# Kernel tuning notes

Hardware: AMD Instinct MI355X
Metric: run time of the kernel (lower is better)

## Reference

```python
import jax, jax.numpy as jnp
import numpy as np

BATCH_K = 8
CUTOFF = 0.5
NONZERO_LOSS_CUTOFF = 1.4
N, D = 8192, 128


def setup_inputs() -> dict:
    key = jax.random.key(0)
    x = jax.random.normal(key, (N, D), dtype=jnp.float32)
    # the sqrt(2 - 2*sim) distance assumes unit-norm embeddings
    x = x / jnp.linalg.norm(x, axis=1, keepdims=True)
    return {"x": x}


def _forward(x, key):
    n, d = x.shape
    k = BATCH_K
    # pairwise distances on the unit sphere
    sim = x @ x.T                                   # [n, n]
    dist = jnp.sqrt(jnp.maximum(2.0 - 2.0 * sim, 0.0))
    # clamp distance from below at cutoff (canonical distance-weighted sampling;
    # repo's clamp(max=) + torch.maxx are typos that make the original code NaN/crash)
    dist = jnp.maximum(dist, CUTOFF)
    one_minus = jnp.maximum(1.0 - 0.25 * dist * dist, 1e-8)  # tiny clip for log safety
    log_w = (2.0 - float(d)) * jnp.log(dist) - (float(d - 3) / 2.0) * jnp.log(one_minus)
    w = jnp.exp(log_w - jnp.max(log_w))
    # zero out the same-class (block-diagonal) entries and far pairs
    blk = jnp.arange(n) // k
    neq_block = (blk[:, None] != blk[None, :]).astype(x.dtype)
    w = w * neq_block * (dist < NONZERO_LOSS_CUTOFF).astype(x.dtype)
    row_sum = jnp.sum(w, axis=1, keepdims=True)
    # uniform fallback for degenerate rows (mirrors the try/except in the original)
    probs = jnp.where(row_sum > 0, w / row_sum, 1.0 / n)   # [n, n]
    # per-row categorical sampling of k-1 negatives WITH replacement
    logits = jnp.log(probs)                                # -inf where prob==0 (ok)
    n_idx = jax.random.categorical(key, logits, shape=(k - 1, n)).T.reshape(-1)  # [n*(k-1)]
    # anchor/positive pairs: all same-block pairs (i, j), j != i
    a_idx = jnp.repeat(jnp.arange(n), k - 1)               # [n*(k-1)]
    p_mat = blk[:, None] * k + jnp.arange(k)[None, :]      # [n, k]
    keep = p_mat != jnp.arange(n)[:, None]
    order = jnp.argsort(jnp.logical_not(keep), axis=1, stable=True)
    p_idx = jnp.take_along_axis(p_mat, order, axis=1)[:, : k - 1].reshape(-1)
    return a_idx, x[a_idx], x[p_idx], x[n_idx], x


def reference(x):
    return _forward(x, jax.random.key(1))
```

## Files before the change

kernel.cpp:

```cpp
#include <hip/hip_runtime.h>

#define NN   8192
#define DD   128
#define KM1  7
#define TPB  256
#define NBLK 512

#define O0_END   57344
#define O1_END   7397376
#define O2_END   14737408
#define O3_END   22077440
#define TOTAL    23126016
#define NKEY     57344

typedef __attribute__((ext_vector_type(8))) short bf16x8;
typedef __attribute__((ext_vector_type(4))) float f32x4;

__device__ __forceinline__ unsigned mix32(unsigned h) {
  h ^= h >> 16; h *= 0x85ebca6bu; h ^= h >> 13; h *= 0xc2b2ae35u; h ^= h >> 16;
  return h;
}

__device__ __forceinline__ float wfun(float dot, int col, int rowblk) {
  float d2m = fmaxf(fmaf(-2.f, dot, 2.f), 0.25f);
  bool vb = ((col >> 3) != rowblk) && (d2m < 1.96f);
  float lgd = __log2f(d2m);
  float om  = fmaf(-0.25f, d2m, 1.f);
  float lgo = __log2f(om);
  float lgw = fmaf(-62.5f, lgo, fmaf(-63.f, lgd, -63.f));
  float w   = __builtin_amdgcn_exp2f(lgw);
  return vb ? w : 0.f;
}

__device__ __forceinline__ float wave_incl_scan(float v, int lane) {
#pragma unroll
  for (int off = 1; off < 64; off <<= 1) {
    float t = __shfl_up(v, off);
    if (lane >= off) v += t;
  }
  return v;
}

__global__ __launch_bounds__(256) void to_bf16(const float4* __restrict__ x4,
                                               ushort4* __restrict__ xb4) {
  const int i = blockIdx.x * 256 + threadIdx.x;
  float4 v = x4[i];
  ushort4 o;
  unsigned u;
  u = __float_as_uint(v.x); o.x = (unsigned short)((u + 0x7FFFu + ((u >> 16) & 1u)) >> 16);
  u = __float_as_uint(v.y); o.y = (unsigned short)((u + 0x7FFFu + ((u >> 16) & 1u)) >> 16);
  u = __float_as_uint(v.z); o.z = (unsigned short)((u + 0x7FFFu + ((u >> 16) & 1u)) >> 16);
  u = __float_as_uint(v.w); o.w = (unsigned short)((u + 0x7FFFu + ((u >> 16) & 1u)) >> 16);
  xb4[i] = o;
}

__global__ __launch_bounds__(TPB, 2) void pass_a(const unsigned short* __restrict__ xb,
                                                 float* __restrict__ bs) {
  const int tid  = threadIdx.x;
  const int lane = tid & 63;
  const int wid  = tid >> 6;
  const int l15  = lane & 15;
  const int g    = lane >> 4;
  const int i0   = ((int)(blockIdx.x >> 5)) * 256 + wid * 64;
  const int oc   = (int)(blockIdx.x & 31);
  const int c0   = oc * 256;
  const int koff = g * 8;

  bf16x8 rw[4][4];
#pragma unroll
  for (int rg = 0; rg < 4; ++rg) {
    const unsigned short* rp = xb + (size_t)(i0 + rg * 16 + l15) * DD + koff;
#pragma unroll
    for (int kk = 0; kk < 4; ++kk)
      rw[rg][kk] = *reinterpret_cast<const bf16x8*>(rp + kk * 32);
  }

  float bsl[16];
#pragma unroll
  for (int j = 0; j < 16; ++j) bsl[j] = 0.f;

#pragma unroll 1
  for (int t = 0; t < 8; ++t) {
    const int ct = c0 + t * 32;
    bf16x8 cf[2][4];
#pragma unroll
    for (int mf = 0; mf < 2; ++mf) {
      const unsigned short* cp = xb + (size_t)(ct + mf * 16 + l15) * DD + koff;
#pragma unroll
      for (int kk = 0; kk < 4; ++kk)
        cf[mf][kk] = *reinterpret_cast<const bf16x8*>(cp + kk * 32);
    }

    f32x4 acc[2][4];
#pragma unroll
    for (int mf = 0; mf < 2; ++mf)
#pragma unroll
      for (int rg = 0; rg < 4; ++rg) acc[mf][rg] = (f32x4){0.f, 0.f, 0.f, 0.f};

#pragma unroll
    for (int mf = 0; mf < 2; ++mf)
#pragma unroll
      for (int rg = 0; rg < 4; ++rg)
#pragma unroll
        for (int kk = 0; kk < 4; ++kk)
          acc[mf][rg] = __builtin_amdgcn_mfma_f32_16x16x32_bf16(cf[mf][kk], rw[rg][kk],
                                                                acc[mf][rg], 0, 0, 0);

#pragma unroll
    for (int mf = 0; mf < 2; ++mf) {
      float s[4];
#pragma unroll
      for (int rg = 0; rg < 4; ++rg) {
        const int rowblk = (i0 + rg * 16 + l15) >> 3;
        float sv = 0.f;
#pragma unroll
        for (int r = 0; r < 4; ++r) {
          const int col = ct + mf * 16 + g * 4 + r;
          sv += wfun(acc[mf][rg][r], col, rowblk);
        }
        sv += __shfl_xor(sv, 16);
        sv += __shfl_xor(sv, 32);
        s[rg] = sv;
      }
      float v = (g == 0) ? s[0] : (g == 1) ? s[1] : (g == 2) ? s[2] : s[3];
      bsl[2 * t + mf] = v;
    }
  }

  float* dst = bs + (size_t)(i0 + lane) * NBLK + oc * 16;
#pragma unroll
  for (int k4 = 0; k4 < 4; ++k4) {
    f32x4 o = {bsl[4 * k4], bsl[4 * k4 + 1], bsl[4 * k4 + 2], bsl[4 * k4 + 3]};
    *reinterpret_cast<f32x4*>(dst + 4 * k4) = o;
  }
}

__global__ __launch_bounds__(TPB) void pass_b(const unsigned short* __restrict__ xb,
                                              const float* __restrict__ bs,
                                              unsigned* __restrict__ nidx) {
  const int lane = threadIdx.x & 63;
  const int wid  = threadIdx.x >> 6;
  const int draw = (int)blockIdx.x * 4 + wid;
  const int row  = draw / KM1;

  const float* bsr = bs + (size_t)row * NBLK;
  float4 v0 = *reinterpret_cast<const float4*>(bsr + lane * 8);
  float4 v1 = *reinterpret_cast<const float4*>(bsr + lane * 8 + 4);
  float s8 = ((v0.x + v0.y) + (v0.z + v0.w)) + ((v1.x + v1.y) + (v1.z + v1.w));
  float pre = wave_incl_scan(s8, lane);
  float W = __shfl(pre, 63);

  unsigned h = mix32((unsigned)draw * 2654435761u + 0x12345u);
  float u = ((float)(h >> 9) + 0.5f) * (1.0f / 8388608.0f);

  if (!(W > 0.f)) {
    if (lane == 0) nidx[draw] = mix32((unsigned)draw * 0x68bc21ebu + 77u) & (NN - 1);
    return;
  }
  float target = u * W;

  unsigned long long ball = __ballot(pre >= target);
  int Lc = ball ? ((int)__ffsll(ball) - 1) : 63;
  float exL = __shfl(pre - s8, Lc);
  float a0 = __shfl(v0.x, Lc), a1 = __shfl(v0.y, Lc), a2 = __shfl(v0.z, Lc),
        a3 = __shfl(v0.w, Lc), a4 = __shfl(v1.x, Lc), a5 = __shfl(v1.y, Lc),
        a6 = __shfl(v1.z, Lc), a7 = __shfl(v1.w, Lc);
  int k = -1; float res = 0.f, bsb = 0.f, c = exL;
#define PICK(j, aj) { float cn = c + (aj); if (k < 0 && cn >= target) { k = j; res = target - c; bsb = (aj); } c = cn; }
  PICK(0, a0) PICK(1, a1) PICK(2, a2) PICK(3, a3)
  PICK(4, a4) PICK(5, a5) PICK(6, a6) PICK(7, a7)
#undef PICK
#define LASTP(j, aj) { if (k < 0 && (aj) > 0.f) { k = j; res = (aj); bsb = (aj); } }
  LASTP(7, a7) LASTP(6, a6) LASTP(5, a5) LASTP(4, a4)
  LASTP(3, a3) LASTP(2, a2) LASTP(1, a1) LASTP(0, a0)
#undef LASTP
  if (k < 0) {
    if (lane == 0) nidx[draw] = mix32((unsigned)draw * 0x68bc21ebu + 77u) & (NN - 1);
    return;
  }
  const int blk = Lc * 8 + k;
  const int cb  = blk * 16;

  const int c_local = lane >> 2;
  const int part    = lane & 3;
  const int col     = cb + c_local;
  const unsigned short* cp = xb + (size_t)col * DD + part * 32;
  const unsigned short* ap = xb + (size_t)row * DD + part * 32;
  float dot = 0.f;
#pragma unroll
  for (int vv = 0; vv < 4; ++vv) {
    bf16x8 cv = *reinterpret_cast<const bf16x8*>(cp + vv * 8);
    bf16x8 av = *reinterpret_cast<const bf16x8*>(ap + vv * 8);
#pragma unroll
    for (int j = 0; j < 8; ++j) {
      float cf = __uint_as_float(((unsigned)(unsigned short)cv[j]) << 16);
      float af = __uint_as_float(((unsigned)(unsigned short)av[j]) << 16);
      dot = fmaf(cf, af, dot);
    }
  }
  dot += __shfl_xor(dot, 1);
  dot += __shfl_xor(dot, 2);
  float w = wfun(dot, col, row >> 3);
  float v = (part == 0) ? w : 0.f;
  float pre2 = wave_incl_scan(v, lane);
  float SW = __shfl(pre2, 63);
  unsigned result;
  if (SW > 0.f) {
    float t2 = (res / bsb) * SW;
    unsigned long long m = __ballot((v > 0.f) && (pre2 >= t2));
    if (m) result = (unsigned)(cb + (((int)__ffsll(m) - 1) >> 2));
    else {
      unsigned long long m2 = __ballot(v > 0.f);
      result = (unsigned)(cb + ((63 - (int)__clzll(m2)) >> 2));
    }
  } else {
    result = mix32((unsigned)draw * 0x68bc21ebu + 77u) & (NN - 1);
  }
  if (lane == 0) nidx[draw] = result;
}

__global__ __launch_bounds__(256) void write_outputs(const float* __restrict__ x,
                                                     const unsigned* __restrict__ nidx,
                                                     float* __restrict__ out) {
  const int qq = blockIdx.x * 256 + threadIdx.x;
  if (qq >= TOTAL / 4) return;
  const int e = qq * 4;
  float4 v;
  if (e < O0_END) {
    v.x = (float)((e    ) / KM1);
    v.y = (float)((e + 1) / KM1);
    v.z = (float)((e + 2) / KM1);
    v.w = (float)((e + 3) / KM1);
  } else if (e < O1_END) {
    int t = e - O0_END; int sidx = t >> 7; int d = t & 127;
    v = *reinterpret_cast<const float4*>(x + (size_t)(sidx / KM1) * DD + d);
  } else if (e < O2_END) {
    int t = e - O1_END; int sidx = t >> 7; int d = t & 127;
    int i = sidx / KM1; int j = sidx - i * KM1; int m = i & 7;
    int p = (i >> 3) * 8 + j + (j >= m ? 1 : 0);
    v = *reinterpret_cast<const float4*>(x + (size_t)p * DD + d);
  } else if (e < O3_END) {
    int t = e - O2_END; int sidx = t >> 7; int d = t & 127;
    int nix = (int)nidx[sidx];
    v = *reinterpret_cast<const float4*>(x + (size_t)nix * DD + d);
  } else {
    v = *reinterpret_cast<const float4*>(x + (e - O3_END));
  }
  f32x4 nv = {v.x, v.y, v.z, v.w};
  __builtin_nontemporal_store(nv, reinterpret_cast<f32x4*>(out + e));
}

extern "C" void kernel_launch(void* const* d_in, const int* in_sizes, int n_in,
                              void* d_out, int out_size, void* d_ws, size_t ws_size,
                              hipStream_t stream) {
  const float* x = (const float*)d_in[0];
  float* out = (float*)d_out;

  float* bs = (float*)d_ws;
  unsigned* nidx = (unsigned*)((char*)d_ws + (size_t)NN * NBLK * 4);
  unsigned short* xb = (unsigned short*)((char*)nidx + NKEY * 4);

  hipLaunchKernelGGL(to_bf16, dim3(NN * DD / 4 / 256), dim3(256), 0, stream,
                     (const float4*)x, (ushort4*)xb);
  hipLaunchKernelGGL(pass_a, dim3(1024), dim3(TPB), 0, stream, xb, bs);
  hipLaunchKernelGGL(pass_b, dim3(NKEY / 4), dim3(TPB), 0, stream, xb, bs, nidx);
  hipLaunchKernelGGL(write_outputs, dim3(TOTAL / 4 / 256), dim3(256), 0, stream,
                     x, nidx, out);
}
```

Before: 113.1 us.

## Exploit Gram-matrix symmetry in pass_a by computing only upper-triangular tile pairs

pass_a now enumerates only the upper-triangular pairs of 128-row chunks (2080 blocks) instead of every row/column tile. Each off-diagonal tile writes its row-direction block sums directly and also reduces the column-direction sums through shuffles and shared memory, then writes them transposed for the mirrored tile. This roughly halves the MFMA work and the weight-function evaluations, at the cost of extra shuffle reductions, a shared-memory transpose, a barrier and a serial loop that decodes the block index into a tile pair.

Measured after the change: 128.6 us. 1.14x slower.

```diff
diff --git a/kernel.cpp b/kernel.cpp
--- a/kernel.cpp
+++ b/kernel.cpp
@@ -5,6 +5,9 @@
 #define KM1  7
 #define TPB  256
 #define NBLK 512
+#define CH   128
+#define NCH  64
+#define NPAIR 2080
 
 #define O0_END   57344
 #define O1_END   7397376
@@ -54,17 +57,22 @@
   xb4[i] = o;
 }
 
-__global__ __launch_bounds__(TPB, 2) void pass_a(const unsigned short* __restrict__ xb,
-                                                 float* __restrict__ bs) {
+__global__ __launch_bounds__(CH, 2) void pass_a(const unsigned short* __restrict__ xb,
+                                                float* __restrict__ bs) {
   const int tid  = threadIdx.x;
   const int lane = tid & 63;
   const int wid  = tid >> 6;
   const int l15  = lane & 15;
   const int g    = lane >> 4;
-  const int i0   = ((int)(blockIdx.x >> 5)) * 256 + wid * 64;
-  const int oc   = (int)(blockIdx.x & 31);
-  const int c0   = oc * 256;
+  int b = (int)blockIdx.x, A = 0;
+  while (b >= NCH - A) { b -= NCH - A; ++A; }
+  const int B  = A + b;
+  const int i0 = A * CH + wid * 64;
+  const int c0 = B * CH;
   const int koff = g * 8;
+  const bool offd = (A != B);
+
+  __shared__ float bsb[CH * 9];
 
   bf16x8 rw[4][4];
 #pragma unroll
@@ -75,12 +83,12 @@
       rw[rg][kk] = *reinterpret_cast<const bf16x8*>(rp + kk * 32);
   }
 
-  float bsl[16];
-#pragma unroll
-  for (int j = 0; j < 16; ++j) bsl[j] = 0.f;
+  float bsl[8];
+#pragma unroll
+  for (int j = 0; j < 8; ++j) bsl[j] = 0.f;
 
 #pragma unroll 1
-  for (int t = 0; t < 8; ++t) {
+  for (int t = 0; t < 4; ++t) {
     const int ct = c0 + t * 32;
     bf16x8 cf[2][4];
 #pragma unroll
@@ -96,7 +104,6 @@
     for (int mf = 0; mf < 2; ++mf)
 #pragma unroll
       for (int rg = 0; rg < 4; ++rg) acc[mf][rg] = (f32x4){0.f, 0.f, 0.f, 0.f};
-
 #pragma unroll
     for (int mf = 0; mf < 2; ++mf)
 #pragma unroll
@@ -106,32 +113,91 @@
           acc[mf][rg] = __builtin_amdgcn_mfma_f32_16x16x32_bf16(cf[mf][kk], rw[rg][kk],
                                                                 acc[mf][rg], 0, 0, 0);
 
+    float w[2][4][4];
+#pragma unroll
+    for (int mf = 0; mf < 2; ++mf)
+#pragma unroll
+      for (int rg = 0; rg < 4; ++rg) {
+        const int rowblk = (i0 + rg * 16 + l15) >> 3;
+#pragma unroll
+        for (int r = 0; r < 4; ++r)
+          w[mf][rg][r] = wfun(acc[mf][rg][r], ct + mf * 16 + g * 4 + r, rowblk);
+      }
+
 #pragma unroll
     for (int mf = 0; mf < 2; ++mf) {
       float s[4];
 #pragma unroll
       for (int rg = 0; rg < 4; ++rg) {
-        const int rowblk = (i0 + rg * 16 + l15) >> 3;
-        float sv = 0.f;
-#pragma unroll
-        for (int r = 0; r < 4; ++r) {
-          const int col = ct + mf * 16 + g * 4 + r;
-          sv += wfun(acc[mf][rg][r], col, rowblk);
-        }
+        float sv = ((w[mf][rg][0] + w[mf][rg][1]) + (w[mf][rg][2] + w[mf][rg][3]));
         sv += __shfl_xor(sv, 16);
         sv += __shfl_xor(sv, 32);
         s[rg] = sv;
       }
-      float v = (g == 0) ? s[0] : (g == 1) ? s[1] : (g == 2) ? s[2] : s[3];
-      bsl[2 * t + mf] = v;
-    }
-  }
-
-  float* dst = bs + (size_t)(i0 + lane) * NBLK + oc * 16;
-#pragma unroll
-  for (int k4 = 0; k4 < 4; ++k4) {
-    f32x4 o = {bsl[4 * k4], bsl[4 * k4 + 1], bsl[4 * k4 + 2], bsl[4 * k4 + 3]};
-    *reinterpret_cast<f32x4*>(dst + 4 * k4) = o;
+      bsl[2 * t + mf] = (g == 0) ? s[0] : (g == 1) ? s[1] : (g == 2) ? s[2] : s[3];
+    }
+
+    if (offd) {
+      float v[32];
+#pragma unroll
+      for (int mf = 0; mf < 2; ++mf)
+#pragma unroll
+        for (int rg = 0; rg < 4; ++rg)
+#pragma unroll
+          for (int r = 0; r < 4; ++r)
+            v[mf * 16 + rg * 4 + r] = w[mf][rg][r];
+#pragma unroll
+      for (int i = 0; i < 16; ++i) {
+        float lo = v[i], hi = v[i + 16];
+        float tlo = __shfl_xor(lo, 1), thi = __shfl_xor(hi, 1);
+        v[i] = (l15 & 1) ? (hi + thi) : (lo + tlo);
+      }
+#pragma unroll
+      for (int i = 0; i < 8; ++i) {
+        float lo = v[i], hi = v[i + 8];
+        float tlo = __shfl_xor(lo, 2), thi = __shfl_xor(hi, 2);
+        v[i] = (l15 & 2) ? (hi + thi) : (lo + tlo);
+      }
+#pragma unroll
+      for (int i = 0; i < 4; ++i) {
+        float lo = v[i], hi = v[i + 4];
+        float tlo = __shfl_xor(lo, 4), thi = __shfl_xor(hi, 4);
+        v[i] = (l15 & 4) ? (hi + thi) : (lo + tlo);
+      }
+#pragma unroll
+      for (int i = 0; i < 2; ++i) {
+        float lo = v[i], hi = v[i + 2];
+        float tlo = __shfl_xor(lo, 8), thi = __shfl_xor(hi, 8);
+        v[i] = (l15 & 8) ? (hi + thi) : (lo + tlo);
+      }
+      const int ib = ((l15 & 1) << 4) | (((l15 >> 1) & 1) << 3) |
+                     (((l15 >> 2) & 1) << 2) | (((l15 >> 3) & 1) << 1);
+#pragma unroll
+      for (int slot = 0; slot < 2; ++slot) {
+        const int idx = ib + slot;
+        const int mf = idx >> 4, rg = (idx >> 2) & 3, r = idx & 3;
+        const int cl = t * 32 + mf * 16 + g * 4 + r;
+        bsb[cl * 9 + wid * 4 + rg] = v[slot];
+      }
+    }
+  }
+
+  {
+    float* dst = bs + (size_t)(i0 + lane) * NBLK + B * 8;
+    f32x4 o0 = {bsl[0], bsl[1], bsl[2], bsl[3]};
+    f32x4 o1 = {bsl[4], bsl[5], bsl[6], bsl[7]};
+    *reinterpret_cast<f32x4*>(dst)     = o0;
+    *reinterpret_cast<f32x4*>(dst + 4) = o1;
+  }
+
+  if (offd) {
+    __syncthreads();
+    const float* src = bsb + tid * 9;
+    float* db = bs + (size_t)(B * CH + tid) * NBLK + A * 8;
+    f32x4 o0 = {src[0], src[1], src[2], src[3]};
+    f32x4 o1 = {src[4], src[5], src[6], src[7]};
+    *reinterpret_cast<f32x4*>(db)     = o0;
+    *reinterpret_cast<f32x4*>(db + 4) = o1;
   }
 }
 
@@ -165,12 +231,12 @@
   float a0 = __shfl(v0.x, Lc), a1 = __shfl(v0.y, Lc), a2 = __shfl(v0.z, Lc),
         a3 = __shfl(v0.w, Lc), a4 = __shfl(v1.x, Lc), a5 = __shfl(v1.y, Lc),
         a6 = __shfl(v1.z, Lc), a7 = __shfl(v1.w, Lc);
-  int k = -1; float res = 0.f, bsb = 0.f, c = exL;
-#define PICK(j, aj) { float cn = c + (aj); if (k < 0 && cn >= target) { k = j; res = target - c; bsb = (aj); } c = cn; }
+  int k = -1; float res = 0.f, bsb2 = 0.f, c = exL;
+#define PICK(j, aj) { float cn = c + (aj); if (k < 0 && cn >= target) { k = j; res = target - c; bsb2 = (aj); } c = cn; }
   PICK(0, a0) PICK(1, a1) PICK(2, a2) PICK(3, a3)
   PICK(4, a4) PICK(5, a5) PICK(6, a6) PICK(7, a7)
 #undef PICK
-#define LASTP(j, aj) { if (k < 0 && (aj) > 0.f) { k = j; res = (aj); bsb = (aj); } }
+#define LASTP(j, aj) { if (k < 0 && (aj) > 0.f) { k = j; res = (aj); bsb2 = (aj); } }
   LASTP(7, a7) LASTP(6, a6) LASTP(5, a5) LASTP(4, a4)
   LASTP(3, a3) LASTP(2, a2) LASTP(1, a1) LASTP(0, a0)
 #undef LASTP
@@ -206,7 +272,7 @@
   float SW = __shfl(pre2, 63);
   unsigned result;
   if (SW > 0.f) {
-    float t2 = (res / bsb) * SW;
+    float t2 = (res / bsb2) * SW;
     unsigned long long m = __ballot((v > 0.f) && (pre2 >= t2));
     if (m) result = (unsigned)(cb + (((int)__ffsll(m) - 1) >> 2));
     else {
@@ -262,7 +328,7 @@
 
   hipLaunchKernelGGL(to_bf16, dim3(NN * DD / 4 / 256), dim3(256), 0, stream,
                      (const float4*)x, (ushort4*)xb);
-  hipLaunchKernelGGL(pass_a, dim3(1024), dim3(TPB), 0, stream, xb, bs);
+  hipLaunchKernelGGL(pass_a, dim3(NPAIR), dim3(CH), 0, stream, xb, bs);
   hipLaunchKernelGGL(pass_b, dim3(NKEY / 4), dim3(TPB), 0, stream, xb, bs, nidx);
   hipLaunchKernelGGL(write_outputs, dim3(TOTAL / 4 / 256), dim3(256), 0, stream,
                      x, nidx, out);
```
